# Kernel optimization log

Hardware: AMD Instinct MI355X
Metric: run time of the kernel (lower is better)

## Reference

```python
import jax, jax.numpy as jnp
import numpy as np


def setup_inputs() -> dict:
    key = jax.random.key(0)
    ks = jax.random.split(key, 8)
    B, N, D, H = 8, 512, 64, 64
    user_embeddings = jax.random.normal(ks[0], (B, N, D), dtype=jnp.float32)
    past_lengths = jax.random.randint(ks[1], (B,), 0, N)
    valid_mask = jnp.ones((B, N), dtype=jnp.float32)
    # MLP params: Linear(4D -> H), PReLU (single slope), Linear(H -> 1)
    s1 = 1.0 / np.sqrt(4 * D)
    s2 = 1.0 / np.sqrt(H)
    W1 = jax.random.uniform(ks[2], (H, 4 * D), minval=-s1, maxval=s1, dtype=jnp.float32)
    b1 = jax.random.uniform(ks[3], (H,), minval=-s1, maxval=s1, dtype=jnp.float32)
    prelu_a = jnp.float32(0.25)
    W2 = jax.random.uniform(ks[4], (1, H), minval=-s2, maxval=s2, dtype=jnp.float32)
    b2 = jax.random.uniform(ks[5], (1,), minval=-s2, maxval=s2, dtype=jnp.float32)
    return {"past_lengths": past_lengths, "user_embeddings": user_embeddings,
            "valid_mask": valid_mask, "W1": W1, "b1": b1, "prelu_a": prelu_a,
            "W2": W2, "b2": b2}


def reference(past_lengths, user_embeddings, valid_mask, W1, b1, prelu_a, W2, b2):
    # DIN local activation attention with causal mask.
    # Original math: h = W1 @ concat(Q, K, Q-K, Q*K) + b1 per (q,k) pair.
    # Split W1 into its 4 D-sized blocks so the concat tensor [B,N,N,4D] is
    # never materialized; the pairwise hidden [B,N,N,H] is the only big buffer.
    B, N, D = user_embeddings.shape
    Wq, Wk, Wd, Wm = jnp.split(W1, 4, axis=1)  # each [H, D]
    x = user_embeddings
    # Q and (Q-K)'s +Q part -> per-query term; K and (Q-K)'s -K part -> per-key term
    hq = jnp.einsum('bqd,hd->bqh', x, Wq + Wd)          # [B,N,H]
    hk = jnp.einsum('bkd,hd->bkh', x, Wk - Wd)          # [B,N,H]
    hm = jnp.einsum('bqd,bkd,hd->bqkh', x, x, Wm)       # [B,N,N,H] (Q*K term)
    h = hq[:, :, None, :] + hk[:, None, :, :] + hm + b1
    h = jnp.where(h > 0, h, prelu_a * h)                # PReLU
    scores = jnp.einsum('bqkh,h->bqk', h, W2[0]) + b2[0]  # [B,N,N]
    causal = jnp.tril(jnp.ones((N, N), dtype=scores.dtype))
    scores = scores * causal[None, :, :]
    scores = scores * valid_mask[:, None, :]            # key-side padding mask
    encoded = jnp.einsum('bqk,bkd->bqd', scores, x)     # weighted sum (no softmax)
    return encoded
```

## Files before the change

### kernel.cpp

```cpp
#include <hip/hip_runtime.h>

#define NB 8
#define NN 512

#define WS_WMF 0
#define WS_HQ  4096
#define WS_BF  266240
#define WS_XE  528384

typedef float fx4 __attribute__((ext_vector_type(4)));
typedef short sx8 __attribute__((ext_vector_type(8)));
typedef int   ix4 __attribute__((ext_vector_type(4)));

static __device__ inline unsigned short f2bf(float f) {
    unsigned u = __float_as_uint(f);
    return (unsigned short)((u + 0x7FFFu + ((u >> 16) & 1u)) >> 16);
}

__global__ __launch_bounds__(256) void prep(const float* __restrict__ x,
                                            const float* __restrict__ vm,
                                            const float* __restrict__ W1,
                                            const float* __restrict__ b1,
                                            float* __restrict__ ws) {
    __shared__ float lwq[64 * 65];
    __shared__ float lwk[64 * 65];
    __shared__ float xs[256];
    const int t = threadIdx.x;
    const int blk = blockIdx.x;

    {
        int d = t & 63, hb = t >> 6;
        #pragma unroll 4
        for (int i = 0; i < 16; ++i) {
            int h = i * 4 + hb;
            float a = W1[h * 256 + d];
            float bb = W1[h * 256 + 64 + d];
            float c = W1[h * 256 + 128 + d];
            lwq[d * 65 + h] = a + c;
            lwk[d * 65 + h] = bb - c;
        }
    }
    const int r0 = blk * 4;
    xs[t] = x[r0 * 64 + t];
    __syncthreads();

    {
        int r = t >> 6, h = t & 63;
        const float* xr = xs + r * 64;
        float aq = b1[h], ak = 0.f;
        #pragma unroll
        for (int dd = 0; dd < 64; ++dd) {
            float xv = xr[dd];
            aq = fmaf(xv, lwq[dd * 65 + h], aq);
            ak = fmaf(xv, lwk[dd * 65 + h], ak);
        }
        int row = r0 + r;
        (ws + WS_HQ)[row * 64 + h] = aq;
        unsigned short* bfp = (unsigned short*)(ws + WS_BF);
        int bb = row >> 9, k = row & 511;
        int tt = k >> 4, nn = k & 15;
        int c = 2 + (h >> 5);
        int qd = (h >> 3) & 3, j = h & 7;
        int ln = qd * 16 + nn;
        bfp[((((bb * 32 + tt) * 4 + c) * 64 + ln) << 3) + j] = f2bf(ak);
    }

    if (blk < 256) {
        int b = blk >> 5, t5 = blk & 31;
        if (t < 128) {
            unsigned short* bfp = (unsigned short*)(ws + WS_BF);
            int c = t >> 6, L = t & 63;
            int nn = L & 15, qd = L >> 4;
            const float* src = x + ((b * 512 + t5 * 16 + nn) * 64 + c * 32 + qd * 8);
            fx4 v0 = *(const fx4*)src;
            fx4 v1 = *(const fx4*)(src + 4);
            uint4 o;
            o.x = (unsigned)f2bf(v0[0]) | ((unsigned)f2bf(v0[1]) << 16);
            o.y = (unsigned)f2bf(v0[2]) | ((unsigned)f2bf(v0[3]) << 16);
            o.z = (unsigned)f2bf(v1[0]) | ((unsigned)f2bf(v1[1]) << 16);
            o.w = (unsigned)f2bf(v1[2]) | ((unsigned)f2bf(v1[3]) << 16);
            *(uint4*)(bfp + ((((b * 32 + t5) * 4 + c) * 64 + L) << 3)) = o;
        }
        {
            unsigned short* xep = (unsigned short*)(ws + WS_XE);
            int c32 = t5 >> 1, half = t5 & 1;
            int nt = t >> 6, r = t & 63;
            int L = half * 32 + (r & 31);
            int j0 = (r >> 5) * 4;
            int quad = L >> 4, nn = L & 15;
            unsigned short u[4];
            #pragma unroll
            for (int i = 0; i < 4; ++i) {
                int key = c32 * 32 + quad * 8 + j0 + i;
                float v = x[(b * 512 + key) * 64 + nt * 16 + nn] * vm[b * 512 + key];
                u[i] = f2bf(v);
            }
            uint2 o;
            o.x = (unsigned)u[0] | ((unsigned)u[1] << 16);
            o.y = (unsigned)u[2] | ((unsigned)u[3] << 16);
            *(uint2*)(xep + (((((b * 16 + c32) * 4 + nt) * 64 + L) << 3) + j0)) = o;
        }
    } else if (blk < 258) {
        float* wmf = ws + WS_WMF;
        int e = (blk - 256) * 256 + t;
        int slot = e >> 6, lane = e & 63;
        int ht = slot >> 1, hf = slot & 1;
        int m = lane & 15, qd = lane >> 4;
        int h = ht * 16 + m;
        int dbase = hf * 32 + qd * 8;
        #pragma unroll
        for (int j = 0; j < 8; ++j)
            wmf[e * 8 + j] = W1[h * 256 + 192 + dbase + j];
    }
}

__global__ __launch_bounds__(256, 2) void k2_main(const float* __restrict__ x,
                                                  const float* __restrict__ prelu_a,
                                                  const float* __restrict__ W2,
                                                  const float* __restrict__ b2,
                                                  const float* __restrict__ ws,
                                                  float* __restrict__ out) {
    const int tid  = threadIdx.x;
    const int lane = tid & 63;
    const int wid  = blockIdx.x * 4 + (tid >> 6);
    const int b    = wid >> 9;
    const int rr   = wid & 511;
    const int q    = (rr & 1) ? (511 - (rr >> 1)) : (rr >> 1);
    const int n    = lane & 15, quad = lane >> 4;
    const int bq   = b * 512 + q;

    const float* wmf = ws + WS_WMF;
    const float* hq  = ws + WS_HQ;
    const unsigned short* bfp = (const unsigned short*)(ws + WS_BF);
    const unsigned short* xep = (const unsigned short*)(ws + WS_XE);

    const float pa  = prelu_a[0];
    const float b2v = b2[0];

    float hqr[4][4], w2r[4][4];
    #pragma unroll
    for (int ht = 0; ht < 4; ++ht) {
        fx4 vh = *(const fx4*)(hq + bq * 64 + ht * 16 + quad * 4);
        fx4 vw = *(const fx4*)(W2 + ht * 16 + quad * 4);
        #pragma unroll
        for (int r = 0; r < 4; ++r) { hqr[ht][r] = vh[r]; w2r[ht][r] = vw[r]; }
    }

    float xq[2][8];
    {
        const float* xp = x + bq * 64 + quad * 8;
        fx4 t0 = *(const fx4*)xp;
        fx4 t1 = *(const fx4*)(xp + 4);
        fx4 t2 = *(const fx4*)(xp + 32);
        fx4 t3 = *(const fx4*)(xp + 36);
        #pragma unroll
        for (int j = 0; j < 4; ++j) {
            xq[0][j] = t0[j]; xq[0][4 + j] = t1[j];
            xq[1][j] = t2[j]; xq[1][4 + j] = t3[j];
        }
    }

    sx8 afrag[4][2];
    #pragma unroll
    for (int ht = 0; ht < 4; ++ht)
        #pragma unroll
        for (int hf = 0; hf < 2; ++hf) {
            const float* wp = wmf + (((ht * 2 + hf) * 64 + lane) << 3);
            fx4 w0 = *(const fx4*)wp;
            fx4 w1 = *(const fx4*)(wp + 4);
            sx8 a;
            #pragma unroll
            for (int j = 0; j < 4; ++j) {
                a[j]     = (short)f2bf(w0[j] * xq[hf][j]);
                a[4 + j] = (short)f2bf(w1[j] * xq[hf][4 + j]);
            }
            afrag[ht][hf] = a;
        }

    sx8 oh[4];
    #pragma unroll
    for (int ht = 0; ht < 4; ++ht) {
        sx8 a;
        #pragma unroll
        for (int j = 0; j < 8; ++j) {
            int hp = (ht >> 1) * 32 + quad * 8 + j;
            a[j] = (hp == ht * 16 + n) ? (short)0x3F80 : (short)0;
        }
        oh[ht] = a;
    }

    int idxs[8];
    #pragma unroll
    for (int j = 0; j < 8; ++j) idxs[j] = ((quad * 8 + j) & 15) << 2;
    const unsigned sel = (quad < 2) ? 0x05040100u : 0x07060302u;

    fx4 eacc[4];
    #pragma unroll
    for (int nt = 0; nt < 4; ++nt) eacc[nt] = (fx4){0.f, 0.f, 0.f, 0.f};

    const int cmax = q >> 5;
    for (int c = 0; c <= cmax; ++c) {
        const unsigned short* fb = bfp + ((((b * 32 + 2 * c) * 4) * 64 + lane) << 3);
        sx8 fa0 = *(const sx8*)(fb);
        sx8 fa1 = *(const sx8*)(fb + 512);
        sx8 fa2 = *(const sx8*)(fb + 1024);
        sx8 fa3 = *(const sx8*)(fb + 1536);
        sx8 fb0 = *(const sx8*)(fb + 2048);
        sx8 fb1 = *(const sx8*)(fb + 2560);
        sx8 fb2 = *(const sx8*)(fb + 3072);
        sx8 fb3 = *(const sx8*)(fb + 3584);
        const unsigned short* fe = xep + ((((b * 16 + c) * 4) * 64 + lane) << 3);
        sx8 e0 = *(const sx8*)(fe);
        sx8 e1 = *(const sx8*)(fe + 512);
        sx8 e2 = *(const sx8*)(fe + 1024);
        sx8 e3 = *(const sx8*)(fe + 1536);

        fx4 accA[4], accB[4];
        #pragma unroll
        for (int ht = 0; ht < 4; ++ht) {
            accA[ht] = (fx4){hqr[ht][0], hqr[ht][1], hqr[ht][2], hqr[ht][3]};
            accB[ht] = accA[ht];
        }
        #pragma unroll
        for (int ht = 0; ht < 4; ++ht) {
            accA[ht] = __builtin_amdgcn_mfma_f32_16x16x32_bf16(afrag[ht][0], fa0, accA[ht], 0, 0, 0);
            accB[ht] = __builtin_amdgcn_mfma_f32_16x16x32_bf16(afrag[ht][0], fb0, accB[ht], 0, 0, 0);
        }
        #pragma unroll
        for (int ht = 0; ht < 4; ++ht) {
            accA[ht] = __builtin_amdgcn_mfma_f32_16x16x32_bf16(afrag[ht][1], fa1, accA[ht], 0, 0, 0);
            accB[ht] = __builtin_amdgcn_mfma_f32_16x16x32_bf16(afrag[ht][1], fb1, accB[ht], 0, 0, 0);
        }
        #pragma unroll
        for (int ht = 0; ht < 4; ++ht) {
            accA[ht] = __builtin_amdgcn_mfma_f32_16x16x32_bf16(oh[ht], (ht < 2) ? fa2 : fa3, accA[ht], 0, 0, 0);
            accB[ht] = __builtin_amdgcn_mfma_f32_16x16x32_bf16(oh[ht], (ht < 2) ? fb2 : fb3, accB[ht], 0, 0, 0);
        }

        float s0 = 0.f, s1 = 0.f;
        #pragma unroll
        for (int ht = 0; ht < 4; ++ht)
            #pragma unroll
            for (int r = 0; r < 4; ++r) {
                float za = accA[ht][r];
                float zb = accB[ht][r];
                s0 = fmaf(w2r[ht][r], fmaf(pa, fminf(za, 0.f), fmaxf(za, 0.f)), s0);
                s1 = fmaf(w2r[ht][r], fmaf(pa, fminf(zb, 0.f), fmaxf(zb, 0.f)), s1);
            }
        s0 += __shfl_xor(s0, 16, 64);
        s0 += __shfl_xor(s0, 32, 64);
        s1 += __shfl_xor(s1, 16, 64);
        s1 += __shfl_xor(s1, 32, 64);
        int k0 = c * 32 + n;
        s0 = (k0 <= q)      ? s0 + b2v : 0.f;
        s1 = (k0 + 16 <= q) ? s1 + b2v : 0.f;

        unsigned packed = (unsigned)f2bf(s0) | ((unsigned)f2bf(s1) << 16);
        int g[8];
        #pragma unroll
        for (int j = 0; j < 8; ++j)
            g[j] = __builtin_amdgcn_ds_bpermute(idxs[j], (int)packed);
        ix4 sw;
        sw[0] = (int)__builtin_amdgcn_perm((unsigned)g[1], (unsigned)g[0], sel);
        sw[1] = (int)__builtin_amdgcn_perm((unsigned)g[3], (unsigned)g[2], sel);
        sw[2] = (int)__builtin_amdgcn_perm((unsigned)g[5], (unsigned)g[4], sel);
        sw[3] = (int)__builtin_amdgcn_perm((unsigned)g[7], (unsigned)g[6], sel);
        sx8 sfrag = __builtin_bit_cast(sx8, sw);

        eacc[0] = __builtin_amdgcn_mfma_f32_16x16x32_bf16(sfrag, e0, eacc[0], 0, 0, 0);
        eacc[1] = __builtin_amdgcn_mfma_f32_16x16x32_bf16(sfrag, e1, eacc[1], 0, 0, 0);
        eacc[2] = __builtin_amdgcn_mfma_f32_16x16x32_bf16(sfrag, e2, eacc[2], 0, 0, 0);
        eacc[3] = __builtin_amdgcn_mfma_f32_16x16x32_bf16(sfrag, e3, eacc[3], 0, 0, 0);
    }

    float ov = eacc[0][0];
    if (quad == 1) ov = eacc[1][0];
    if (quad == 2) ov = eacc[2][0];
    if (quad == 3) ov = eacc[3][0];
    out[bq * 64 + quad * 16 + n] = ov;
}

extern "C" void kernel_launch(void* const* d_in, const int* in_sizes, int n_in,
                              void* d_out, int out_size, void* d_ws, size_t ws_size,
                              hipStream_t stream) {
    const float* x   = (const float*)d_in[1];
    const float* vmk = (const float*)d_in[2];
    const float* W1  = (const float*)d_in[3];
    const float* b1  = (const float*)d_in[4];
    const float* pa  = (const float*)d_in[5];
    const float* W2  = (const float*)d_in[6];
    const float* b2  = (const float*)d_in[7];
    float* ws  = (float*)d_ws;
    float* out = (float*)d_out;

    hipLaunchKernelGGL(prep, dim3(NB * NN / 4), dim3(256), 0, stream,
                       x, vmk, W1, b1, ws);
    hipLaunchKernelGGL(k2_main, dim3(NB * NN / 4), dim3(256), 0, stream,
                       x, pa, W2, b2, ws, out);
}
```

Before: 121.8 us.

## Split score and aggregation into two loops staged through shared memory

The main loop now only computes the pairwise MLP scores and writes packed bf16 score pairs into a per-wave shared-memory buffer. A second loop then reads them back as MFMA fragments and runs the score-times-embedding accumulation. This replaces eight ds_bpermute cross-lane shuffles per chunk with LDS stores and vector loads, and moves the embedding-fragment loads out of the score loop. The PReLU is also rewritten as max(z, a*z) with split accumulators to shorten dependency chains, which is only equivalent when the slope is at most 1. The cost is 4 KB of extra LDS per block and a second pass over the chunks.

```diff
diff --git a/kernel.cpp b/kernel.cpp
--- a/kernel.cpp
+++ b/kernel.cpp
@@ -122,7 +122,8 @@
                                                   float* __restrict__ out) {
     const int tid  = threadIdx.x;
     const int lane = tid & 63;
-    const int wid  = blockIdx.x * 4 + (tid >> 6);
+    const int w    = tid >> 6;
+    const int wid  = blockIdx.x * 4 + w;
     const int b    = wid >> 9;
     const int rr   = wid & 511;
     const int q    = (rr & 1) ? (511 - (rr >> 1)) : (rr >> 1);
@@ -136,6 +137,9 @@
 
     const float pa  = prelu_a[0];
     const float b2v = b2[0];
+
+    __shared__ unsigned sjoint[4 * 256];
+    unsigned* myS = sjoint + w * 256;
 
     float hqr[4][4], w2r[4][4];
     #pragma unroll
@@ -189,16 +193,8 @@
         oh[ht] = a;
     }
 
-    int idxs[8];
-    #pragma unroll
-    for (int j = 0; j < 8; ++j) idxs[j] = ((quad * 8 + j) & 15) << 2;
-    const unsigned sel = (quad < 2) ? 0x05040100u : 0x07060302u;
-
-    fx4 eacc[4];
-    #pragma unroll
-    for (int nt = 0; nt < 4; ++nt) eacc[nt] = (fx4){0.f, 0.f, 0.f, 0.f};
-
     const int cmax = q >> 5;
+
     for (int c = 0; c <= cmax; ++c) {
         const unsigned short* fb = bfp + ((((b * 32 + 2 * c) * 4) * 64 + lane) << 3);
         sx8 fa0 = *(const sx8*)(fb);
@@ -209,11 +205,6 @@
         sx8 fb1 = *(const sx8*)(fb + 2560);
         sx8 fb2 = *(const sx8*)(fb + 3072);
         sx8 fb3 = *(const sx8*)(fb + 3584);
-        const unsigned short* fe = xep + ((((b * 16 + c) * 4) * 64 + lane) << 3);
-        sx8 e0 = *(const sx8*)(fe);
-        sx8 e1 = *(const sx8*)(fe + 512);
-        sx8 e2 = *(const sx8*)(fe + 1024);
-        sx8 e3 = *(const sx8*)(fe + 1536);
 
         fx4 accA[4], accB[4];
         #pragma unroll
@@ -237,16 +228,24 @@
             accB[ht] = __builtin_amdgcn_mfma_f32_16x16x32_bf16(oh[ht], (ht < 2) ? fb2 : fb3, accB[ht], 0, 0, 0);
         }
 
-        float s0 = 0.f, s1 = 0.f;
-        #pragma unroll
-        for (int ht = 0; ht < 4; ++ht)
+        float s0a = 0.f, s0b = 0.f, s1a = 0.f, s1b = 0.f;
+        #pragma unroll
+        for (int ht = 0; ht < 2; ++ht)
             #pragma unroll
             for (int r = 0; r < 4; ++r) {
-                float za = accA[ht][r];
-                float zb = accB[ht][r];
-                s0 = fmaf(w2r[ht][r], fmaf(pa, fminf(za, 0.f), fmaxf(za, 0.f)), s0);
-                s1 = fmaf(w2r[ht][r], fmaf(pa, fminf(zb, 0.f), fmaxf(zb, 0.f)), s1);
+                float za = accA[ht][r], zb = accB[ht][r];
+                s0a = fmaf(w2r[ht][r], fmaxf(za, za * pa), s0a);
+                s1a = fmaf(w2r[ht][r], fmaxf(zb, zb * pa), s1a);
             }
+        #pragma unroll
+        for (int ht = 2; ht < 4; ++ht)
+            #pragma unroll
+            for (int r = 0; r < 4; ++r) {
+                float za = accA[ht][r], zb = accB[ht][r];
+                s0b = fmaf(w2r[ht][r], fmaxf(za, za * pa), s0b);
+                s1b = fmaf(w2r[ht][r], fmaxf(zb, zb * pa), s1b);
+            }
+        float s0 = s0a + s0b, s1 = s1a + s1b;
         s0 += __shfl_xor(s0, 16, 64);
         s0 += __shfl_xor(s0, 32, 64);
         s1 += __shfl_xor(s1, 16, 64);
@@ -256,16 +255,30 @@
         s1 = (k0 + 16 <= q) ? s1 + b2v : 0.f;
 
         unsigned packed = (unsigned)f2bf(s0) | ((unsigned)f2bf(s1) << 16);
-        int g[8];
-        #pragma unroll
-        for (int j = 0; j < 8; ++j)
-            g[j] = __builtin_amdgcn_ds_bpermute(idxs[j], (int)packed);
+        if (quad == 0) myS[c * 16 + n] = packed;
+    }
+
+    const unsigned sel = (quad < 2) ? 0x05040100u : 0x07060302u;
+    fx4 eacc[4];
+    #pragma unroll
+    for (int nt = 0; nt < 4; ++nt) eacc[nt] = (fx4){0.f, 0.f, 0.f, 0.f};
+
+    for (int c = 0; c <= cmax; ++c) {
+        const unsigned* sp = myS + c * 16 + (quad & 1) * 8;
+        uint4 wv0 = *(const uint4*)sp;
+        uint4 wv1 = *(const uint4*)(sp + 4);
         ix4 sw;
-        sw[0] = (int)__builtin_amdgcn_perm((unsigned)g[1], (unsigned)g[0], sel);
-        sw[1] = (int)__builtin_amdgcn_perm((unsigned)g[3], (unsigned)g[2], sel);
-        sw[2] = (int)__builtin_amdgcn_perm((unsigned)g[5], (unsigned)g[4], sel);
-        sw[3] = (int)__builtin_amdgcn_perm((unsigned)g[7], (unsigned)g[6], sel);
+        sw[0] = (int)__builtin_amdgcn_perm(wv0.y, wv0.x, sel);
+        sw[1] = (int)__builtin_amdgcn_perm(wv0.w, wv0.z, sel);
+        sw[2] = (int)__builtin_amdgcn_perm(wv1.y, wv1.x, sel);
+        sw[3] = (int)__builtin_amdgcn_perm(wv1.w, wv1.z, sel);
         sx8 sfrag = __builtin_bit_cast(sx8, sw);
+
+        const unsigned short* fe = xep + ((((b * 16 + c) * 4) * 64 + lane) << 3);
+        sx8 e0 = *(const sx8*)(fe);
+        sx8 e1 = *(const sx8*)(fe + 512);
+        sx8 e2 = *(const sx8*)(fe + 1024);
+        sx8 e3 = *(const sx8*)(fe + 1536);
 
         eacc[0] = __builtin_amdgcn_mfma_f32_16x16x32_bf16(sfrag, e0, eacc[0], 0, 0, 0);
         eacc[1] = __builtin_amdgcn_mfma_f32_16x16x32_bf16(sfrag, e1, eacc[1], 0, 0, 0);
```

New measurement: 120.3 us. Within noise of the previous version (-1.2%).
